# Performance work log

Hardware: AMD Instinct MI355X
Metric: run time of the kernel (lower is better)

The kernel has to match this reference:

```python
import jax, jax.numpy as jnp
import numpy as np

VOCAB = 8192  # upper bound on integer values appearing in features


def setup_inputs() -> dict:
    key = jax.random.key(0)
    # [B, L] integer codes; each row is treated as a SET of values (duplicates ignored)
    features = jax.random.randint(key, (4096, 256), 0, VOCAB, dtype=jnp.int32)
    return {"features": features}


def reference(features) -> jnp.ndarray:
    # np.intersect1d / np.union1d compute set intersection/union of unique values.
    # Equivalent vectorized form: binary presence matrix P[i, v] = 1 iff value v in row i.
    B, L = features.shape
    rows = jnp.arange(B)[:, None]                                  # [B, 1]
    presence = jnp.zeros((B, VOCAB), jnp.float32).at[rows, features].set(1.0)  # [B, V]
    inter = presence @ presence.T                                  # [B, B] |A_i & A_j|
    sizes = presence.sum(axis=1)                                   # [B]    |A_i|
    union = sizes[:, None] + sizes[None, :] - inter                # [B, B] |A_i | A_j|
    # original returns -intersection/union (note the negation), 0 when union == 0
    sim = jnp.where(union != 0, -inter / jnp.where(union != 0, union, 1.0), 0.0)
    return sim
```

## Files before the change

kernel.cpp:

```cpp
#include <hip/hip_runtime.h>
#include <hip/hip_bf16.h>
#include <stdint.h>

#define B_ROWS 4096
#define L_FEAT 256
#define VOCAB  8192

#define BM 128
#define BN 128
#define BK 64

typedef __attribute__((ext_vector_type(4))) int   intx4;
typedef __attribute__((ext_vector_type(4))) float floatx4;

__device__ __forceinline__ void async_copy16(const void* gsrc, void* ldst) {
  __builtin_amdgcn_global_load_lds(
      (const __attribute__((address_space(1))) void*)gsrc,
      (__attribute__((address_space(3))) void*)ldst, 16, 0, 0);
}

__global__ void zero_kernel(uint4* __restrict__ p, int n16) {
  int i = blockIdx.x * blockDim.x + threadIdx.x;
  const int stride = gridDim.x * blockDim.x;
  const uint4 z = make_uint4(0u, 0u, 0u, 0u);
  for (; i < n16; i += stride) p[i] = z;
}

__global__ void scatter_kernel(const int* __restrict__ f,
                               unsigned char* __restrict__ P) {
  const int id  = blockIdx.x * 256 + threadIdx.x;
  const int row = id >> 8;
  const int v   = f[id];
  P[(size_t)row * VOCAB + v] = 1;
}

__global__ void sizes_kernel(const uint4* __restrict__ P4,
                             float* __restrict__ sizes) {
  const int row = blockIdx.x;
  const uint4* rp = P4 + (size_t)row * (VOCAB / 16);
  int cnt = 0;
  for (int j = threadIdx.x; j < VOCAB / 16; j += 256) {
    uint4 x = rp[j];
    cnt += __popc(x.x) + __popc(x.y) + __popc(x.z) + __popc(x.w);
  }
  #pragma unroll
  for (int off = 32; off > 0; off >>= 1) cnt += __shfl_down(cnt, off);
  __shared__ int ws[4];
  if ((threadIdx.x & 63) == 0) ws[threadIdx.x >> 6] = cnt;
  __syncthreads();
  if (threadIdx.x == 0)
    sizes[row] = (float)(ws[0] + ws[1] + ws[2] + ws[3]);
}

__global__ __launch_bounds__(256) void gemm_kernel(
    const unsigned char* __restrict__ P,
    const float* __restrict__ sizes,
    float* __restrict__ out) {
  int b = blockIdx.x, by = 0, rem = 32;
  while (b >= rem) { b -= rem; ++by; --rem; }
  const int bx = by + b;
  const int iBase = by * BM;
  const int jBase = bx * BN;

  __shared__ __align__(16) unsigned char As[BM * BK];
  __shared__ __align__(16) unsigned char Bs[BN * BK];

  const int tid  = threadIdx.x;
  const int wave = tid >> 6, lane = tid & 63;
  const int wm = wave >> 1, wn = wave & 1;
  const int col16 = lane & 15, quad = lane >> 4;

  intx4 acc[4][4];
  #pragma unroll
  for (int a = 0; a < 4; ++a)
    #pragma unroll
    for (int c = 0; c < 4; ++c) acc[a][c] = (intx4){0, 0, 0, 0};

  const int srow = lane >> 2;
  const int scol = (lane & 3) * 16;

  for (int k0 = 0; k0 < VOCAB; k0 += BK) {
    __syncthreads();
    #pragma unroll
    for (int t = 0; t < 2; ++t) {
      const int c = wave + t * 4;
      const int r = c * 16 + srow;
      async_copy16(P + (size_t)(iBase + r) * VOCAB + k0 + scol, &As[c * 1024]);
      async_copy16(P + (size_t)(jBase + r) * VOCAB + k0 + scol, &Bs[c * 1024]);
    }
    __syncthreads();

    intx4 a[4], bfr[4];
    #pragma unroll
    for (int tm = 0; tm < 4; ++tm)
      a[tm] = *(const intx4*)&As[(wm * 64 + tm * 16 + col16) * BK + quad * 16];
    #pragma unroll
    for (int tn = 0; tn < 4; ++tn)
      bfr[tn] = *(const intx4*)&Bs[(wn * 64 + tn * 16 + col16) * BK + quad * 16];
    #pragma unroll
    for (int tm = 0; tm < 4; ++tm)
      #pragma unroll
      for (int tn = 0; tn < 4; ++tn)
        acc[tm][tn] = __builtin_amdgcn_mfma_i32_16x16x64_i8(
            a[tm], bfr[tn], acc[tm][tn], 0, 0, 0);
  }

  #pragma unroll
  for (int tm = 0; tm < 4; ++tm) {
    #pragma unroll
    for (int tn = 0; tn < 4; ++tn) {
      const int col = jBase + wn * 64 + tn * 16 + col16;
      const float sj = sizes[col];
      #pragma unroll
      for (int r = 0; r < 4; ++r) {
        const int row = iBase + wm * 64 + tm * 16 + quad * 4 + r;
        const float inter = (float)acc[tm][tn][r];
        const float u = sizes[row] + sj - inter;
        out[(size_t)row * B_ROWS + col] = (u != 0.f) ? (-inter / u) : 0.f;
      }
    }
  }
}

__global__ void mirror_kernel(float* __restrict__ out) {
  const int bx = blockIdx.x, by = blockIdx.y;
  if (bx >= by) return;
  const int rBase = by * 128, cBase = bx * 128;
  __shared__ float tile[32][33];
  const int tx = threadIdx.x & 31, ty8 = threadIdx.x >> 5;
  for (int s = 0; s < 16; ++s) {
    const int si = s >> 2, sj = s & 3;
    #pragma unroll
    for (int k = 0; k < 4; ++k) {
      const int sr = ty8 + k * 8;
      tile[sr][tx] =
          out[(size_t)(cBase + sj * 32 + sr) * B_ROWS + rBase + si * 32 + tx];
    }
    __syncthreads();
    #pragma unroll
    for (int k = 0; k < 4; ++k) {
      const int dr = ty8 + k * 8;
      out[(size_t)(rBase + si * 32 + dr) * B_ROWS + cBase + sj * 32 + tx] =
          tile[tx][dr];
    }
    __syncthreads();
  }
}

extern "C" void kernel_launch(void* const* d_in, const int* in_sizes, int n_in,
                              void* d_out, int out_size, void* d_ws, size_t ws_size,
                              hipStream_t stream) {
  const int* features = (const int*)d_in[0];
  float* out = (float*)d_out;
  unsigned char* P = (unsigned char*)d_ws;
  float* sizes = (float*)((char*)d_ws + (size_t)B_ROWS * VOCAB);

  zero_kernel<<<2048, 256, 0, stream>>>((uint4*)P, B_ROWS * VOCAB / 16);
  scatter_kernel<<<(B_ROWS * L_FEAT) / 256, 256, 0, stream>>>(features, P);
  sizes_kernel<<<B_ROWS, 256, 0, stream>>>((const uint4*)P, sizes);
  gemm_kernel<<<528, 256, 0, stream>>>(P, sizes, out);
  mirror_kernel<<<dim3(32, 32), 256, 0, stream>>>(out);
}
```

Baseline: 199.0 us.

## Split-K the triangular int8 GEMM into u16 partials with combine and fused epilogue

The upper-triangle GEMM now runs over two K slabs (doubling the grid from 528 to 1056 blocks for better CU occupancy) and writes 16-bit partial intersection counts into the output buffer as scratch. A combine kernel sums the two partials into a workspace buffer, and a new epilogue kernel computes the Jaccard values for both triangles, replacing the separate mirror pass. LDS reads and writes also get an XOR-like rotation to reduce bank conflicts. This adds extra kernel launches and scratch traffic, and the lower-triangle epilogue reads transposed u16 data with strided, uncoalesced accesses.

```diff
diff --git a/kernel.cpp b/kernel.cpp
--- a/kernel.cpp
+++ b/kernel.cpp
@@ -9,14 +9,20 @@
 #define BM 128
 #define BN 128
 #define BK 64
-
-typedef __attribute__((ext_vector_type(4))) int   intx4;
-typedef __attribute__((ext_vector_type(4))) float floatx4;
+#define NTILE 32
+#define NTRI  528
+#define KSPLIT 4096
+
+typedef __attribute__((ext_vector_type(4))) int intx4;
 
 __device__ __forceinline__ void async_copy16(const void* gsrc, void* ldst) {
   __builtin_amdgcn_global_load_lds(
       (const __attribute__((address_space(1))) void*)gsrc,
       (__attribute__((address_space(3))) void*)ldst, 16, 0, 0);
+}
+
+__device__ __forceinline__ int tri_index(int a, int b) {
+  return a * NTILE - (a * (a - 1)) / 2 + (b - a);
 }
 
 __global__ void zero_kernel(uint4* __restrict__ p, int n16) {
@@ -54,9 +60,9 @@
 
 __global__ __launch_bounds__(256) void gemm_kernel(
     const unsigned char* __restrict__ P,
-    const float* __restrict__ sizes,
-    float* __restrict__ out) {
-  int b = blockIdx.x, by = 0, rem = 32;
+    unsigned short* __restrict__ scratch) {
+  const int tile = blockIdx.x, slab = blockIdx.y;
+  int b = tile, by = 0, rem = NTILE;
   while (b >= rem) { b -= rem; ++by; --rem; }
   const int bx = by + b;
   const int iBase = by * BM;
@@ -77,9 +83,12 @@
     for (int c = 0; c < 4; ++c) acc[a][c] = (intx4){0, 0, 0, 0};
 
   const int srow = lane >> 2;
-  const int scol = (lane & 3) * 16;
-
-  for (int k0 = 0; k0 < VOCAB; k0 += BK) {
+  const int scol = ((((lane & 3) - ((lane >> 3) & 3)) & 3) * 16);
+  const int rdoff = (((quad + (col16 >> 1)) & 3) * 16);
+
+  const int k0base = slab * KSPLIT;
+  for (int kk = 0; kk < KSPLIT; kk += BK) {
+    const int k0 = k0base + kk;
     __syncthreads();
     #pragma unroll
     for (int t = 0; t < 2; ++t) {
@@ -93,10 +102,10 @@
     intx4 a[4], bfr[4];
     #pragma unroll
     for (int tm = 0; tm < 4; ++tm)
-      a[tm] = *(const intx4*)&As[(wm * 64 + tm * 16 + col16) * BK + quad * 16];
+      a[tm] = *(const intx4*)&As[(wm * 64 + tm * 16 + col16) * BK + rdoff];
     #pragma unroll
     for (int tn = 0; tn < 4; ++tn)
-      bfr[tn] = *(const intx4*)&Bs[(wn * 64 + tn * 16 + col16) * BK + quad * 16];
+      bfr[tn] = *(const intx4*)&Bs[(wn * 64 + tn * 16 + col16) * BK + rdoff];
     #pragma unroll
     for (int tm = 0; tm < 4; ++tm)
       #pragma unroll
@@ -105,45 +114,72 @@
             a[tm], bfr[tn], acc[tm][tn], 0, 0, 0);
   }
 
+  unsigned short* pp = scratch + ((size_t)slab * NTRI + tile) * (BM * BN);
   #pragma unroll
-  for (int tm = 0; tm < 4; ++tm) {
+  for (int tm = 0; tm < 4; ++tm)
     #pragma unroll
     for (int tn = 0; tn < 4; ++tn) {
-      const int col = jBase + wn * 64 + tn * 16 + col16;
-      const float sj = sizes[col];
+      const int colL = wn * 64 + tn * 16 + col16;
       #pragma unroll
       for (int r = 0; r < 4; ++r) {
-        const int row = iBase + wm * 64 + tm * 16 + quad * 4 + r;
-        const float inter = (float)acc[tm][tn][r];
-        const float u = sizes[row] + sj - inter;
-        out[(size_t)row * B_ROWS + col] = (u != 0.f) ? (-inter / u) : 0.f;
+        const int rowL = wm * 64 + tm * 16 + quad * 4 + r;
+        pp[rowL * BN + colL] = (unsigned short)acc[tm][tn][r];
       }
     }
-  }
-}
-
-__global__ void mirror_kernel(float* __restrict__ out) {
+}
+
+__global__ void combine_kernel(const uint4* __restrict__ scratch,
+                               uint4* __restrict__ summed) {
+  const int tile = blockIdx.x;
+  const uint4* s0 = scratch + (size_t)tile * (BM * BN / 8);
+  const uint4* s1 = scratch + ((size_t)NTRI + tile) * (BM * BN / 8);
+  uint4* d = summed + (size_t)tile * (BM * BN / 8);
+  for (int k = 0; k < 8; ++k) {
+    const int idx = threadIdx.x + k * 256;
+    uint4 a = s0[idx], b = s1[idx];
+    a.x += b.x; a.y += b.y; a.z += b.z; a.w += b.w;
+    d[idx] = a;
+  }
+}
+
+__global__ void epilogue_kernel(const unsigned short* __restrict__ summed,
+                                const float* __restrict__ sizes,
+                                float* __restrict__ out) {
   const int bx = blockIdx.x, by = blockIdx.y;
-  if (bx >= by) return;
-  const int rBase = by * 128, cBase = bx * 128;
-  __shared__ float tile[32][33];
-  const int tx = threadIdx.x & 31, ty8 = threadIdx.x >> 5;
-  for (int s = 0; s < 16; ++s) {
-    const int si = s >> 2, sj = s & 3;
-    #pragma unroll
-    for (int k = 0; k < 4; ++k) {
-      const int sr = ty8 + k * 8;
-      tile[sr][tx] =
-          out[(size_t)(cBase + sj * 32 + sr) * B_ROWS + rBase + si * 32 + tx];
-    }
-    __syncthreads();
-    #pragma unroll
-    for (int k = 0; k < 4; ++k) {
-      const int dr = ty8 + k * 8;
-      out[(size_t)(rBase + si * 32 + dr) * B_ROWS + cBase + sj * 32 + tx] =
-          tile[tx][dr];
-    }
-    __syncthreads();
+  const int tid = threadIdx.x;
+  const int r  = tid >> 1;
+  const int ch = tid & 1;
+  const int R = by * BM + r;
+  const float si = sizes[R];
+  float* orow = out + (size_t)R * B_ROWS + bx * BN + ch * 64;
+
+  if (bx >= by) {
+    const unsigned short* u = summed + (size_t)tri_index(by, bx) * (BM * BN);
+    const uint4* up = (const uint4*)(u + r * BN + ch * 64);
+    #pragma unroll
+    for (int k = 0; k < 8; ++k) {
+      uint4 w = up[k];
+      unsigned int ww[4] = {w.x, w.y, w.z, w.w};
+      #pragma unroll
+      for (int q = 0; q < 4; ++q) {
+        const int cbase = bx * BN + ch * 64 + k * 8 + q * 2;
+        const float i0 = (float)(ww[q] & 0xFFFFu);
+        const float i1 = (float)(ww[q] >> 16);
+        const float u0 = si + sizes[cbase]     - i0;
+        const float u1 = si + sizes[cbase + 1] - i1;
+        orow[k * 8 + q * 2]     = (u0 != 0.f) ? (-i0 / u0) : 0.f;
+        orow[k * 8 + q * 2 + 1] = (u1 != 0.f) ? (-i1 / u1) : 0.f;
+      }
+    }
+  } else {
+    const unsigned short* u = summed + (size_t)tri_index(bx, by) * (BM * BN);
+    #pragma unroll 8
+    for (int i = 0; i < 64; ++i) {
+      const int cL = ch * 64 + i;
+      const float iv = (float)u[cL * BN + r];
+      const float uv = si + sizes[bx * BN + cL] - iv;
+      orow[i] = (uv != 0.f) ? (-iv / uv) : 0.f;
+    }
   }
 }
 
@@ -154,10 +190,14 @@
   float* out = (float*)d_out;
   unsigned char* P = (unsigned char*)d_ws;
   float* sizes = (float*)((char*)d_ws + (size_t)B_ROWS * VOCAB);
+  unsigned short* summed =
+      (unsigned short*)((char*)d_ws + (size_t)B_ROWS * VOCAB + 16384);
+  unsigned short* scratch = (unsigned short*)d_out;
 
   zero_kernel<<<2048, 256, 0, stream>>>((uint4*)P, B_ROWS * VOCAB / 16);
   scatter_kernel<<<(B_ROWS * L_FEAT) / 256, 256, 0, stream>>>(features, P);
   sizes_kernel<<<B_ROWS, 256, 0, stream>>>((const uint4*)P, sizes);
-  gemm_kernel<<<528, 256, 0, stream>>>(P, sizes, out);
-  mirror_kernel<<<dim3(32, 32), 256, 0, stream>>>(out);
-}
+  gemm_kernel<<<dim3(NTRI, 2), 256, 0, stream>>>(P, scratch);
+  combine_kernel<<<NTRI, 256, 0, stream>>>((const uint4*)scratch, (uint4*)summed);
+  epilogue_kernel<<<dim3(NTILE, NTILE), 256, 0, stream>>>(summed, sizes, out);
+}
```

Measured after the change: 302.8 us. 1.52x slower.

## Bit-pack presence matrix in tiled layout and expand to int8 in registers for MFMA

Applied to the files above, without the earlier changes.

The byte-per-entry presence matrix is replaced by a bit-packed matrix stored in a tile-blocked layout, built with atomicOr. The GEMM loads 64-bit words straight into registers and expands each bit to an int8 lane with byte permutes, so shared-memory staging is gone and operand traffic drops by 8x. The epilogue stages the counts in LDS, writes both the tile and its transpose with vectorized stores, and drops the separate mirror kernel. In exchange it adds ALU work for bit expansion, atomics in the scatter, and register-level prefetch with a tighter launch bound. The union != 0 guard is also dropped.

```diff
diff --git a/kernel.cpp b/kernel.cpp
--- a/kernel.cpp
+++ b/kernel.cpp
@@ -1,23 +1,15 @@
 #include <hip/hip_runtime.h>
-#include <hip/hip_bf16.h>
 #include <stdint.h>
 
 #define B_ROWS 4096
 #define L_FEAT 256
 #define VOCAB  8192
 
-#define BM 128
-#define BN 128
-#define BK 64
+#define NTILE 32
+#define NTRI  528
+#define NKP   128
 
-typedef __attribute__((ext_vector_type(4))) int   intx4;
-typedef __attribute__((ext_vector_type(4))) float floatx4;
-
-__device__ __forceinline__ void async_copy16(const void* gsrc, void* ldst) {
-  __builtin_amdgcn_global_load_lds(
-      (const __attribute__((address_space(1))) void*)gsrc,
-      (__attribute__((address_space(3))) void*)ldst, 16, 0, 0);
-}
+typedef __attribute__((ext_vector_type(4))) int intx4;
 
 __global__ void zero_kernel(uint4* __restrict__ p, int n16) {
   int i = blockIdx.x * blockDim.x + threadIdx.x;
@@ -27,123 +19,149 @@
 }
 
 __global__ void scatter_kernel(const int* __restrict__ f,
-                               unsigned char* __restrict__ P) {
-  const int id  = blockIdx.x * 256 + threadIdx.x;
-  const int row = id >> 8;
-  const int v   = f[id];
-  P[(size_t)row * VOCAB + v] = 1;
+                               unsigned int* __restrict__ Pk) {
+  const int id = blockIdx.x * 256 + threadIdx.x;
+  const int r  = id >> 8;
+  const int v  = f[id];
+  const int w  = (((r >> 7) * NKP + (v >> 6)) * 128 + (r & 127)) * 2 +
+                 ((v >> 5) & 1);
+  atomicOr(&Pk[w], 1u << (v & 31));
 }
 
-__global__ void sizes_kernel(const uint4* __restrict__ P4,
+__global__ void sizes_kernel(const uint2* __restrict__ Pk2,
                              float* __restrict__ sizes) {
-  const int row = blockIdx.x;
-  const uint4* rp = P4 + (size_t)row * (VOCAB / 16);
+  const int g  = blockIdx.x;
+  const int rl = threadIdx.x & 127;
+  const int h  = threadIdx.x >> 7;
+  const uint2* p = Pk2 + ((size_t)g * NKP + h * 64) * 128 + rl;
   int cnt = 0;
-  for (int j = threadIdx.x; j < VOCAB / 16; j += 256) {
-    uint4 x = rp[j];
-    cnt += __popc(x.x) + __popc(x.y) + __popc(x.z) + __popc(x.w);
+  #pragma unroll 8
+  for (int kp = 0; kp < 64; ++kp) {
+    const uint2 v = p[(size_t)kp * 128];
+    cnt += __popc(v.x) + __popc(v.y);
   }
-  #pragma unroll
-  for (int off = 32; off > 0; off >>= 1) cnt += __shfl_down(cnt, off);
-  __shared__ int ws[4];
-  if ((threadIdx.x & 63) == 0) ws[threadIdx.x >> 6] = cnt;
+  __shared__ int part[128];
+  if (h == 0) part[rl] = cnt;
   __syncthreads();
-  if (threadIdx.x == 0)
-    sizes[row] = (float)(ws[0] + ws[1] + ws[2] + ws[3]);
+  if (h == 1) sizes[g * 128 + rl] = (float)(part[rl] + cnt);
 }
 
-__global__ __launch_bounds__(256) void gemm_kernel(
-    const unsigned char* __restrict__ P,
+__device__ __forceinline__ intx4 expand16(uint2 v, bool hi, unsigned sel0,
+                                          unsigned sel1) {
+  const unsigned w  = hi ? v.y : v.x;
+  const unsigned r0 = __builtin_amdgcn_perm(w, w, sel0);
+  const unsigned r1 = __builtin_amdgcn_perm(w, w, sel1);
+  intx4 f;
+  f[0] = (int)(((r0 & 0x08040201u) + 0x7f7f7f7fu) & 0x80808080u);
+  f[1] = (int)(((r0 & 0x80402010u) + 0x7f7f7f7fu) & 0x80808080u);
+  f[2] = (int)(((r1 & 0x08040201u) + 0x7f7f7f7fu) & 0x80808080u);
+  f[3] = (int)(((r1 & 0x80402010u) + 0x7f7f7f7fu) & 0x80808080u);
+  return f;
+}
+
+__global__ __launch_bounds__(256, 3) void gemm_kernel(
+    const uint2* __restrict__ Pk2,
     const float* __restrict__ sizes,
     float* __restrict__ out) {
-  int b = blockIdx.x, by = 0, rem = 32;
-  while (b >= rem) { b -= rem; ++by; --rem; }
-  const int bx = by + b;
-  const int iBase = by * BM;
-  const int jBase = bx * BN;
-
-  __shared__ __align__(16) unsigned char As[BM * BK];
-  __shared__ __align__(16) unsigned char Bs[BN * BK];
+  int t = blockIdx.x, a = 0, rem = NTILE;
+  while (t >= rem) { t -= rem; ++a; --rem; }
+  const int b = a + t;
 
   const int tid  = threadIdx.x;
   const int wave = tid >> 6, lane = tid & 63;
   const int wm = wave >> 1, wn = wave & 1;
   const int col16 = lane & 15, quad = lane >> 4;
 
+  const bool hi = (quad & 2) != 0;
+  const unsigned sel0 = 0x01010101u * (unsigned)((quad & 1) * 2);
+  const unsigned sel1 = sel0 + 0x01010101u;
+
+  const uint2* pa = Pk2 + (size_t)a * (NKP * 128) + wm * 64 + col16;
+  const uint2* pb = Pk2 + (size_t)b * (NKP * 128) + wn * 64 + col16;
+
   intx4 acc[4][4];
   #pragma unroll
-  for (int a = 0; a < 4; ++a)
+  for (int i = 0; i < 4; ++i)
     #pragma unroll
-    for (int c = 0; c < 4; ++c) acc[a][c] = (intx4){0, 0, 0, 0};
+    for (int j = 0; j < 4; ++j) acc[i][j] = (intx4){0, 0, 0, 0};
 
-  const int srow = lane >> 2;
-  const int scol = (lane & 3) * 16;
+  uint2 va[4], vb[4];
+  #pragma unroll
+  for (int m = 0; m < 4; ++m) { va[m] = pa[m * 16]; vb[m] = pb[m * 16]; }
+  pa += 128; pb += 128;
 
-  for (int k0 = 0; k0 < VOCAB; k0 += BK) {
-    __syncthreads();
+  for (int it = 0; it < NKP; ++it) {
+    uint2 na[4], nb[4];
     #pragma unroll
-    for (int t = 0; t < 2; ++t) {
-      const int c = wave + t * 4;
-      const int r = c * 16 + srow;
-      async_copy16(P + (size_t)(iBase + r) * VOCAB + k0 + scol, &As[c * 1024]);
-      async_copy16(P + (size_t)(jBase + r) * VOCAB + k0 + scol, &Bs[c * 1024]);
+    for (int m = 0; m < 4; ++m) { na[m] = pa[m * 16]; nb[m] = pb[m * 16]; }
+    pa += 128; pb += 128;
+
+    intx4 af[4];
+    #pragma unroll
+    for (int m = 0; m < 4; ++m) af[m] = expand16(va[m], hi, sel0, sel1);
+    #pragma unroll
+    for (int n = 0; n < 4; ++n) {
+      const intx4 bf = expand16(vb[n], hi, sel0, sel1);
+      #pragma unroll
+      for (int m = 0; m < 4; ++m)
+        acc[m][n] = __builtin_amdgcn_mfma_i32_16x16x64_i8(af[m], bf, acc[m][n],
+                                                          0, 0, 0);
     }
-    __syncthreads();
-
-    intx4 a[4], bfr[4];
     #pragma unroll
-    for (int tm = 0; tm < 4; ++tm)
-      a[tm] = *(const intx4*)&As[(wm * 64 + tm * 16 + col16) * BK + quad * 16];
-    #pragma unroll
-    for (int tn = 0; tn < 4; ++tn)
-      bfr[tn] = *(const intx4*)&Bs[(wn * 64 + tn * 16 + col16) * BK + quad * 16];
-    #pragma unroll
-    for (int tm = 0; tm < 4; ++tm)
-      #pragma unroll
-      for (int tn = 0; tn < 4; ++tn)
-        acc[tm][tn] = __builtin_amdgcn_mfma_i32_16x16x64_i8(
-            a[tm], bfr[tn], acc[tm][tn], 0, 0, 0);
+    for (int m = 0; m < 4; ++m) { va[m] = na[m]; vb[m] = nb[m]; }
   }
 
+  __shared__ unsigned short tile[128][130];
+  __shared__ float rsz[128], csz[128];
+
+  if (tid < 128) rsz[tid] = sizes[a * 128 + tid];
+  else           csz[tid - 128] = sizes[b * 128 + (tid - 128)];
+
   #pragma unroll
-  for (int tm = 0; tm < 4; ++tm) {
+  for (int m = 0; m < 4; ++m)
     #pragma unroll
-    for (int tn = 0; tn < 4; ++tn) {
-      const int col = jBase + wn * 64 + tn * 16 + col16;
-      const float sj = sizes[col];
+    for (int n = 0; n < 4; ++n) {
+      const int col = wn * 64 + n * 16 + col16;
       #pragma unroll
       for (int r = 0; r < 4; ++r) {
-        const int row = iBase + wm * 64 + tm * 16 + quad * 4 + r;
-        const float inter = (float)acc[tm][tn][r];
-        const float u = sizes[row] + sj - inter;
-        out[(size_t)row * B_ROWS + col] = (u != 0.f) ? (-inter / u) : 0.f;
+        const int row = wm * 64 + m * 16 + quad * 4 + r;
+        tile[row][col] = (unsigned short)(((unsigned int)acc[m][n][r]) >> 14);
       }
     }
+  __syncthreads();
+
+  {
+    const int c4 = (tid & 31) * 4;
+    const int r0 = tid >> 5;
+    #pragma unroll
+    for (int rr = 0; rr < 16; ++rr) {
+      const int r = rr * 8 + r0;
+      const float si = rsz[r];
+      float4 o;
+      float iv;
+      iv = (float)tile[r][c4];     o.x = -iv / (si + csz[c4]     - iv);
+      iv = (float)tile[r][c4 + 1]; o.y = -iv / (si + csz[c4 + 1] - iv);
+      iv = (float)tile[r][c4 + 2]; o.z = -iv / (si + csz[c4 + 2] - iv);
+      iv = (float)tile[r][c4 + 3]; o.w = -iv / (si + csz[c4 + 3] - iv);
+      *(float4*)&out[(size_t)(a * 128 + r) * B_ROWS + b * 128 + c4] = o;
+    }
   }
-}
 
-__global__ void mirror_kernel(float* __restrict__ out) {
-  const int bx = blockIdx.x, by = blockIdx.y;
-  if (bx >= by) return;
-  const int rBase = by * 128, cBase = bx * 128;
-  __shared__ float tile[32][33];
-  const int tx = threadIdx.x & 31, ty8 = threadIdx.x >> 5;
-  for (int s = 0; s < 16; ++s) {
-    const int si = s >> 2, sj = s & 3;
+  if (b > a) {
+    const int i4 = (tid & 31) * 4;
+    const int j0 = tid >> 5;
     #pragma unroll
-    for (int k = 0; k < 4; ++k) {
-      const int sr = ty8 + k * 8;
-      tile[sr][tx] =
-          out[(size_t)(cBase + sj * 32 + sr) * B_ROWS + rBase + si * 32 + tx];
+    for (int rr = 0; rr < 16; ++rr) {
+      const int jj = rr * 8 + j0;
+      const float sj = csz[jj];
+      float4 o;
+      float iv;
+      iv = (float)tile[i4][jj];     o.x = -iv / (rsz[i4]     + sj - iv);
+      iv = (float)tile[i4 + 1][jj]; o.y = -iv / (rsz[i4 + 1] + sj - iv);
+      iv = (float)tile[i4 + 2][jj]; o.z = -iv / (rsz[i4 + 2] + sj - iv);
+      iv = (float)tile[i4 + 3][jj]; o.w = -iv / (rsz[i4 + 3] + sj - iv);
+      *(float4*)&out[(size_t)(b * 128 + jj) * B_ROWS + a * 128 + i4] = o;
     }
-    __syncthreads();
-    #pragma unroll
-    for (int k = 0; k < 4; ++k) {
-      const int dr = ty8 + k * 8;
-      out[(size_t)(rBase + si * 32 + dr) * B_ROWS + cBase + sj * 32 + tx] =
-          tile[tx][dr];
-    }
-    __syncthreads();
   }
 }
 
@@ -152,12 +170,11 @@
                               hipStream_t stream) {
   const int* features = (const int*)d_in[0];
   float* out = (float*)d_out;
-  unsigned char* P = (unsigned char*)d_ws;
-  float* sizes = (float*)((char*)d_ws + (size_t)B_ROWS * VOCAB);
+  unsigned int* Pk = (unsigned int*)d_ws;
+  float* sizes = (float*)((char*)d_ws + (size_t)NTILE * NKP * 128 * 8);
 
-  zero_kernel<<<2048, 256, 0, stream>>>((uint4*)P, B_ROWS * VOCAB / 16);
-  scatter_kernel<<<(B_ROWS * L_FEAT) / 256, 256, 0, stream>>>(features, P);
-  sizes_kernel<<<B_ROWS, 256, 0, stream>>>((const uint4*)P, sizes);
-  gemm_kernel<<<528, 256, 0, stream>>>(P, sizes, out);
-  mirror_kernel<<<dim3(32, 32), 256, 0, stream>>>(out);
+  zero_kernel<<<512, 256, 0, stream>>>((uint4*)Pk, NTILE * NKP * 128 * 8 / 16);
+  scatter_kernel<<<(B_ROWS * L_FEAT) / 256, 256, 0, stream>>>(features, Pk);
+  sizes_kernel<<<NTILE, 256, 0, stream>>>((const uint2*)Pk, sizes);
+  gemm_kernel<<<NTRI, 256, 0, stream>>>((const uint2*)Pk, sizes, out);
 }
```

After: 241.1 us. +21.1%, slower.
